# Kernel optimization log

Measured on AMD Instinct MI355X. Metric: run time of the kernel, lower is better.

Reference implementation:

```python
import jax, jax.numpy as jnp
import numpy as np

N, K, C = 200000, 27, 64


def setup_inputs() -> dict:
    key = jax.random.key(0)
    k1, k2, k3, k4 = jax.random.split(key, 4)
    data = jax.random.normal(k1, (N, C), dtype=jnp.float32)
    # Xavier-like scale for depthwise weights (kdim, 1, C)
    weights = jax.random.normal(k2, (K, 1, C), dtype=jnp.float32) * 0.1
    neigh = jax.random.randint(k3, (N, K), 0, N, dtype=jnp.int32)
    invalid = jax.random.uniform(k4, (N, K)) < 0.05
    neigh = jnp.where(invalid, -1, neigh)
    return {"data": data, "weights": weights, "neigh": neigh}


def reference(data, weights, neigh):
    # buffer[i,k,c] = data[neigh[i,k], c] if neigh[i,k] >= 0 else 0
    valid = neigh >= 0                                   # [N, K]
    gathered = jnp.where(valid[:, :, None],
                         data[jnp.clip(neigh, 0)],       # [N, K, C]
                         jnp.zeros((), dtype=data.dtype))
    w = weights.reshape(K, C)                            # flatten(0,1)
    out = jnp.einsum('ikc,kc->ic', gathered, w)          # depthwise conv
    return out
```

## Files before the change

kernel.cpp:

```cpp
#include <hip/hip_runtime.h>
#include <stdint.h>


typedef float    v4f __attribute__((ext_vector_type(4)));
typedef uint32_t v4u __attribute__((ext_vector_type(4)));

constexpr int K   = 27;
constexpr int C   = 64;
constexpr int RPB = 32;

__device__ inline uint32_t bf16pack(float lo, float hi) {
    uint32_t a = __float_as_uint(lo);
    uint32_t b = __float_as_uint(hi);
    a = (a + 0x7FFFu + ((a >> 16) & 1u)) >> 16;
    b = (b + 0x7FFFu + ((b >> 16) & 1u)) & 0xFFFF0000u;
    return a | b;
}

__global__ __launch_bounds__(256) void convert_kernel(
    const v4f* __restrict__ in,
    v4u*       __restrict__ outq,
    int n8)
{
    const int i = blockIdx.x * 256 + threadIdx.x;
    if (i >= n8) return;
    v4f a = __builtin_nontemporal_load(in + 2 * i);
    v4f b = __builtin_nontemporal_load(in + 2 * i + 1);
    v4u q;
    q.x = bf16pack(a.x, a.y);
    q.y = bf16pack(a.z, a.w);
    q.z = bf16pack(b.x, b.y);
    q.w = bf16pack(b.z, b.w);
    outq[i] = q;
}

__global__ __launch_bounds__(256) void gather_kernel(
    const v4u*   __restrict__ dataq,
    const float* __restrict__ weights,
    const int*   __restrict__ neigh,
    v4f*         __restrict__ out4,
    int nrows)
{
    __shared__ float w_lds[K * C];
    __shared__ int   n_lds[RPB * K];

    const int tid = threadIdx.x;
    for (int idx = tid; idx < K * C / 4; idx += 256)
        ((v4f*)w_lds)[idx] = ((const v4f*)weights)[idx];

    const long nbase = (long)blockIdx.x * RPB * K;
    const long ntot  = (long)nrows * K;
    for (int idx = tid; idx < RPB * K; idx += 256) {
        const long g = nbase + idx;
        n_lds[idx] = (g < ntot) ? __builtin_nontemporal_load(neigh + g) : -1;
    }
    __syncthreads();

    const int l     = tid & 7;
    const int group = tid >> 3;
    const int row   = blockIdx.x * RPB + group;
    if (row >= nrows) return;

    const int* __restrict__ nrow = n_lds + group * K;

    v4f acc0 = (v4f){0.f, 0.f, 0.f, 0.f};
    v4f acc1 = (v4f){0.f, 0.f, 0.f, 0.f};

    #pragma unroll
    for (int b = 0; b < K; b += 9) {
        int nk[9];
        v4u d[9];
        #pragma unroll
        for (int j = 0; j < 9; ++j) nk[j] = nrow[b + j];
        #pragma unroll
        for (int j = 0; j < 9; ++j) {
            const int n = nk[j];
            d[j] = dataq[(n < 0 ? 0 : n) * 8 + l];
        }
        #pragma unroll
        for (int j = 0; j < 9; ++j) {
            if (nk[j] < 0) d[j] = (v4u){0u, 0u, 0u, 0u};
            const int k = b + j;
            const v4f* wv = (const v4f*)(w_lds + k * C + l * 8);
            const v4f w0 = wv[0];
            const v4f w1 = wv[1];
            acc0.x += __uint_as_float(d[j].x << 16)          * w0.x;
            acc0.y += __uint_as_float(d[j].x & 0xFFFF0000u)  * w0.y;
            acc0.z += __uint_as_float(d[j].y << 16)          * w0.z;
            acc0.w += __uint_as_float(d[j].y & 0xFFFF0000u)  * w0.w;
            acc1.x += __uint_as_float(d[j].z << 16)          * w1.x;
            acc1.y += __uint_as_float(d[j].z & 0xFFFF0000u)  * w1.y;
            acc1.z += __uint_as_float(d[j].w << 16)          * w1.z;
            acc1.w += __uint_as_float(d[j].w & 0xFFFF0000u)  * w1.w;
        }
    }

    v4f* o = out4 + row * (C / 4) + l * 2;
    __builtin_nontemporal_store(acc0, o);
    __builtin_nontemporal_store(acc1, o + 1);
}

extern "C" void kernel_launch(void* const* d_in, const int* in_sizes, int n_in,
                              void* d_out, int out_size, void* d_ws, size_t ws_size,
                              hipStream_t stream) {
    const float* data    = (const float*)d_in[0];
    const float* weights = (const float*)d_in[1];
    const int*   neigh   = (const int*)d_in[2];
    v4f*         out4    = (v4f*)d_out;
    v4u*         dataq   = (v4u*)d_ws;

    const int nrows = in_sizes[0] / C;
    const int n8    = nrows * C / 8;

    convert_kernel<<<(n8 + 255) / 256, 256, 0, stream>>>(
        (const v4f*)data, dataq, n8);

    const int blocks = (nrows + RPB - 1) / RPB;
    gather_kernel<<<blocks, 256, 0, stream>>>(
        dataq, weights, neigh, out4, nrows);
}
```

Before: 202.3 us.

## Use persistent grid-stride loops for the convert and gather kernels

Both kernels now run as persistent grid-stride loops. The convert kernel is capped at 2048 blocks and each thread packs one float4 into a bf16 pair. The gather kernel runs on 1250 blocks, each looping over row groups, and loads the weights into LDS once per block instead of once per 32 rows. This cuts per-block setup and launch overhead, but the extra barriers reduce latency hiding between groups and may leave some blocks doing more work than others.

```diff
diff --git a/kernel.cpp b/kernel.cpp
--- a/kernel.cpp
+++ b/kernel.cpp
@@ -4,6 +4,7 @@
 
 typedef float    v4f __attribute__((ext_vector_type(4)));
 typedef uint32_t v4u __attribute__((ext_vector_type(4)));
+typedef uint32_t v2u __attribute__((ext_vector_type(2)));
 
 constexpr int K   = 27;
 constexpr int C   = 64;
@@ -19,19 +20,17 @@
 
 __global__ __launch_bounds__(256) void convert_kernel(
     const v4f* __restrict__ in,
-    v4u*       __restrict__ outq,
-    int n8)
+    v2u*       __restrict__ outq,
+    int n4)
 {
-    const int i = blockIdx.x * 256 + threadIdx.x;
-    if (i >= n8) return;
-    v4f a = __builtin_nontemporal_load(in + 2 * i);
-    v4f b = __builtin_nontemporal_load(in + 2 * i + 1);
-    v4u q;
-    q.x = bf16pack(a.x, a.y);
-    q.y = bf16pack(a.z, a.w);
-    q.z = bf16pack(b.x, b.y);
-    q.w = bf16pack(b.z, b.w);
-    outq[i] = q;
+    const int stride = gridDim.x * 256;
+    for (int i = blockIdx.x * 256 + threadIdx.x; i < n4; i += stride) {
+        v4f a = __builtin_nontemporal_load(in + i);
+        v2u q;
+        q.x = bf16pack(a.x, a.y);
+        q.y = bf16pack(a.z, a.w);
+        outq[i] = q;
+    }
 }
 
 __global__ __launch_bounds__(256) void gather_kernel(
@@ -39,7 +38,8 @@
     const float* __restrict__ weights,
     const int*   __restrict__ neigh,
     v4f*         __restrict__ out4,
-    int nrows)
+    int nrows,
+    int ngroups)
 {
     __shared__ float w_lds[K * C];
     __shared__ int   n_lds[RPB * K];
@@ -48,56 +48,61 @@
     for (int idx = tid; idx < K * C / 4; idx += 256)
         ((v4f*)w_lds)[idx] = ((const v4f*)weights)[idx];
 
-    const long nbase = (long)blockIdx.x * RPB * K;
-    const long ntot  = (long)nrows * K;
-    for (int idx = tid; idx < RPB * K; idx += 256) {
-        const long g = nbase + idx;
-        n_lds[idx] = (g < ntot) ? __builtin_nontemporal_load(neigh + g) : -1;
-    }
-    __syncthreads();
-
     const int l     = tid & 7;
     const int group = tid >> 3;
-    const int row   = blockIdx.x * RPB + group;
-    if (row >= nrows) return;
+    const int ntot  = nrows * K;
 
-    const int* __restrict__ nrow = n_lds + group * K;
+    for (int g = blockIdx.x; g < ngroups; g += gridDim.x) {
+        __syncthreads();
+        const int nbase = g * (RPB * K);
+        for (int idx = tid; idx < RPB * K; idx += 256) {
+            const int p = nbase + idx;
+            n_lds[idx] = (p < ntot) ? __builtin_nontemporal_load(neigh + p)
+                                    : -1;
+        }
+        __syncthreads();
 
-    v4f acc0 = (v4f){0.f, 0.f, 0.f, 0.f};
-    v4f acc1 = (v4f){0.f, 0.f, 0.f, 0.f};
+        const int row = g * RPB + group;
+        const int* __restrict__ nrow = n_lds + group * K;
 
-    #pragma unroll
-    for (int b = 0; b < K; b += 9) {
-        int nk[9];
-        v4u d[9];
+        v4f acc0 = (v4f){0.f, 0.f, 0.f, 0.f};
+        v4f acc1 = (v4f){0.f, 0.f, 0.f, 0.f};
+
         #pragma unroll
-        for (int j = 0; j < 9; ++j) nk[j] = nrow[b + j];
-        #pragma unroll
-        for (int j = 0; j < 9; ++j) {
-            const int n = nk[j];
-            d[j] = dataq[(n < 0 ? 0 : n) * 8 + l];
+        for (int b = 0; b < K; b += 9) {
+            int nk[9];
+            v4u d[9];
+            #pragma unroll
+            for (int j = 0; j < 9; ++j) nk[j] = nrow[b + j];
+            #pragma unroll
+            for (int j = 0; j < 9; ++j) {
+                const int n = nk[j];
+                d[j] = dataq[(n < 0 ? 0 : n) * 8 + l];
+            }
+            #pragma unroll
+            for (int j = 0; j < 9; ++j) {
+                if (nk[j] < 0) d[j] = (v4u){0u, 0u, 0u, 0u};
+                const int k = b + j;
+                const v4f* wv = (const v4f*)(w_lds + k * C + l * 8);
+                const v4f w0 = wv[0];
+                const v4f w1 = wv[1];
+                acc0.x += __uint_as_float(d[j].x << 16)          * w0.x;
+                acc0.y += __uint_as_float(d[j].x & 0xFFFF0000u)  * w0.y;
+                acc0.z += __uint_as_float(d[j].y << 16)          * w0.z;
+                acc0.w += __uint_as_float(d[j].y & 0xFFFF0000u)  * w0.w;
+                acc1.x += __uint_as_float(d[j].z << 16)          * w1.x;
+                acc1.y += __uint_as_float(d[j].z & 0xFFFF0000u)  * w1.y;
+                acc1.z += __uint_as_float(d[j].w << 16)          * w1.z;
+                acc1.w += __uint_as_float(d[j].w & 0xFFFF0000u)  * w1.w;
+            }
         }
-        #pragma unroll
-        for (int j = 0; j < 9; ++j) {
-            if (nk[j] < 0) d[j] = (v4u){0u, 0u, 0u, 0u};
-            const int k = b + j;
-            const v4f* wv = (const v4f*)(w_lds + k * C + l * 8);
-            const v4f w0 = wv[0];
-            const v4f w1 = wv[1];
-            acc0.x += __uint_as_float(d[j].x << 16)          * w0.x;
-            acc0.y += __uint_as_float(d[j].x & 0xFFFF0000u)  * w0.y;
-            acc0.z += __uint_as_float(d[j].y << 16)          * w0.z;
-            acc0.w += __uint_as_float(d[j].y & 0xFFFF0000u)  * w0.w;
-            acc1.x += __uint_as_float(d[j].z << 16)          * w1.x;
-            acc1.y += __uint_as_float(d[j].z & 0xFFFF0000u)  * w1.y;
-            acc1.z += __uint_as_float(d[j].w << 16)          * w1.z;
-            acc1.w += __uint_as_float(d[j].w & 0xFFFF0000u)  * w1.w;
+
+        if (row < nrows) {
+            v4f* o = out4 + row * (C / 4) + l * 2;
+            __builtin_nontemporal_store(acc0, o);
+            __builtin_nontemporal_store(acc1, o + 1);
         }
     }
-
-    v4f* o = out4 + row * (C / 4) + l * 2;
-    __builtin_nontemporal_store(acc0, o);
-    __builtin_nontemporal_store(acc1, o + 1);
 }
 
 extern "C" void kernel_launch(void* const* d_in, const int* in_sizes, int n_in,
@@ -107,15 +112,19 @@
     const float* weights = (const float*)d_in[1];
     const int*   neigh   = (const int*)d_in[2];
     v4f*         out4    = (v4f*)d_out;
-    v4u*         dataq   = (v4u*)d_ws;
+    const v4u*   dataq   = (const v4u*)d_ws;
 
     const int nrows = in_sizes[0] / C;
-    const int n8    = nrows * C / 8;
+    const int n4    = nrows * C / 4;
 
-    convert_kernel<<<(n8 + 255) / 256, 256, 0, stream>>>(
-        (const v4f*)data, dataq, n8);
+    int cblocks = (n4 + 255) / 256;
+    if (cblocks > 2048) cblocks = 2048;
+    convert_kernel<<<cblocks, 256, 0, stream>>>(
+        (const v4f*)data, (v2u*)d_ws, n4);
 
-    const int blocks = (nrows + RPB - 1) / RPB;
-    gather_kernel<<<blocks, 256, 0, stream>>>(
-        dataq, weights, neigh, out4, nrows);
+    const int ngroups = (nrows + RPB - 1) / RPB;
+    int gblocks = 1250;
+    if (gblocks > ngroups) gblocks = ngroups;
+    gather_kernel<<<gblocks, 256, 0, stream>>>(
+        dataq, weights, neigh, out4, nrows, ngroups);
 }
```

Measured after the change: 203.6 us. About the same (+0.6%).
